# Performance work log

Measured on AMD Instinct MI355X. Metric: run time of the kernel, lower is better.

The kernel has to match this reference:

```python
import jax, jax.numpy as jnp
import numpy as np

N = 4096
BATCH = 8192


def setup_inputs() -> dict:
    key = jax.random.key(0)
    x = jax.random.normal(key, (BATCH, N), dtype=jnp.float32)
    return {"x": x}


def reference(x):
    # Radix-2 butterfly network (Fast Walsh-Hadamard Transform):
    # at stage s, positions i and i ^ (2**s) are combined as (a+b, a-b).
    B, n = x.shape
    num_stages = int(np.log2(n))
    r = x
    for stage in range(num_stages):  # fixed small loop over log2(n) stages
        stride = 2 ** stage
        # pairs (i, i+stride) live in blocks of 2*stride
        r4 = r.reshape(B, n // (2 * stride), 2, stride)
        a = r4[:, :, 0, :]
        b = r4[:, :, 1, :]
        r = jnp.stack([a + b, a - b], axis=2).reshape(B, n)
    return r
```

## Files before the change

### kernel.cpp

```cpp
#include <hip/hip_runtime.h>


#define N 4096

__device__ __forceinline__ void h16(float r[16]) {
    #pragma unroll
    for (int s = 1; s < 16; s <<= 1) {
        #pragma unroll
        for (int m = 0; m < 16; ++m) {
            if (!(m & s)) {
                float x = r[m], y = r[m ^ s];
                r[m]     = x + y;
                r[m ^ s] = x - y;
            }
        }
    }
}

__global__ __launch_bounds__(256, 8) void fwht4096_kernel(const float* __restrict__ in,
                                                          float* __restrict__ out) {
    __shared__ float lds[N];

    const int t = threadIdx.x;
    const long long row = blockIdx.x;
    const float* __restrict__ rowIn  = in  + row * (long long)N;
    float* __restrict__       rowOut = out + row * (long long)N;

    float r[16];

    #pragma unroll
    for (int j = 0; j < 4; ++j) {
        const float4 v = *reinterpret_cast<const float4*>(rowIn + t * 16 + j * 4);
        r[j * 4 + 0] = v.x; r[j * 4 + 1] = v.y;
        r[j * 4 + 2] = v.z; r[j * 4 + 3] = v.w;
    }

    h16(r);

    const int x = (t >> 4) & 1;
    const int s = (t >> 1) & 3;
    float* wbase = &lds[16 * (t ^ x)];
    #pragma unroll
    for (int c = 0; c < 4; ++c) {
        const int i0 = 4 * (c ^ s);
        const float4 v = make_float4(r[i0], r[i0 + 1], r[i0 + 2], r[i0 + 3]);
        *reinterpret_cast<float4*>(wbase + 4 * c) = v;
    }
    __syncthreads();

    {
        const int chi = t >> 4, a = t & 15;
        const int base = 256 * chi + a;
        const int fx = (chi & 1) << 4;
        #pragma unroll
        for (int k = 0; k < 16; ++k)
            r[k] = lds[(base + 16 * k) ^ fx ^ (((k >> 1) & 3) << 2)];
        h16(r);
        #pragma unroll
        for (int k = 0; k < 16; ++k)
            lds[(base + 16 * k) ^ fx ^ (((k >> 1) & 3) << 2)] = r[k];
    }
    __syncthreads();

    {
        const int b = t >> 4, a = t & 15;
        const int base = 16 * b + a;
        const int fb = ((b >> 1) & 3) << 2;
        #pragma unroll
        for (int k = 0; k < 16; ++k)
            r[k] = lds[(256 * k + base) ^ ((k & 1) << 4) ^ fb];
        h16(r);
        #pragma unroll
        for (int k = 0; k < 16; ++k)
            rowOut[k * 256 + t] = r[k];
    }
}

extern "C" void kernel_launch(void* const* d_in, const int* in_sizes, int n_in,
                              void* d_out, int out_size, void* d_ws, size_t ws_size,
                              hipStream_t stream) {
    const float* x = (const float*)d_in[0];
    float* y = (float*)d_out;
    const int rows = in_sizes[0] / N;
    fwht4096_kernel<<<rows, 256, 0, stream>>>(x, y);
}
```

Measured before the change: 228.2 us.

## Process four rows per block with register prefetch of next row

Each block now handles four rows in sequence and loads the next row's input into a second register set while the current row is transformed, so global load latency overlaps with compute. Barriers are replaced by a custom LDS-only waitcnt plus s_barrier, which avoids waiting on outstanding global loads, and the LDS swizzle indexing is precomputed. In exchange the grid is four times smaller, register pressure rises with the extra 16-float buffer, and the launch assumes rows divide evenly by four.

```diff
diff --git a/kernel.cpp b/kernel.cpp
--- a/kernel.cpp
+++ b/kernel.cpp
@@ -1,7 +1,8 @@
 #include <hip/hip_runtime.h>
 
 
-#define N 4096
+#define NN 4096
+#define RPB 4
 
 __device__ __forceinline__ void h16(float r[16]) {
     #pragma unroll
@@ -17,62 +18,76 @@
     }
 }
 
+__device__ __forceinline__ void lgkm_barrier() {
+    asm volatile("s_waitcnt lgkmcnt(0)" ::: "memory");
+    __builtin_amdgcn_s_barrier();
+    asm volatile("" ::: "memory");
+}
+
 __global__ __launch_bounds__(256, 8) void fwht4096_kernel(const float* __restrict__ in,
                                                           float* __restrict__ out) {
-    __shared__ float lds[N];
+    __shared__ float lds[NN];
 
-    const int t = threadIdx.x;
-    const long long row = blockIdx.x;
-    const float* __restrict__ rowIn  = in  + row * (long long)N;
-    float* __restrict__       rowOut = out + row * (long long)N;
+    const int t   = threadIdx.x;
+    const int chi = t >> 4;
 
-    float r[16];
+    const int wbase = (16 * t) ^ ((t & 7) << 2) ^ (((t >> 4) & 1) << 4);
+    const int tb    = (256 * chi + (t & 15)) ^ ((chi & 1) << 4);
+    const int tc    = t ^ ((chi & 7) << 2);
+
+    const long long row0 = (long long)blockIdx.x * RPB;
+    const float* __restrict__ pin = in + row0 * NN + t * 16;
+
+    float r[16], rn[16];
 
     #pragma unroll
     for (int j = 0; j < 4; ++j) {
-        const float4 v = *reinterpret_cast<const float4*>(rowIn + t * 16 + j * 4);
-        r[j * 4 + 0] = v.x; r[j * 4 + 1] = v.y;
-        r[j * 4 + 2] = v.z; r[j * 4 + 3] = v.w;
+        const float4 v = *reinterpret_cast<const float4*>(pin + 4 * j);
+        r[4*j+0] = v.x; r[4*j+1] = v.y; r[4*j+2] = v.z; r[4*j+3] = v.w;
     }
 
-    h16(r);
+    for (int it = 0; it < RPB; ++it) {
+        if (it + 1 < RPB) {
+            const float* __restrict__ pn = pin + (long long)(it + 1) * NN;
+            #pragma unroll
+            for (int j = 0; j < 4; ++j) {
+                const float4 v = *reinterpret_cast<const float4*>(pn + 4 * j);
+                rn[4*j+0] = v.x; rn[4*j+1] = v.y; rn[4*j+2] = v.z; rn[4*j+3] = v.w;
+            }
+        }
 
-    const int x = (t >> 4) & 1;
-    const int s = (t >> 1) & 3;
-    float* wbase = &lds[16 * (t ^ x)];
-    #pragma unroll
-    for (int c = 0; c < 4; ++c) {
-        const int i0 = 4 * (c ^ s);
-        const float4 v = make_float4(r[i0], r[i0 + 1], r[i0 + 2], r[i0 + 3]);
-        *reinterpret_cast<float4*>(wbase + 4 * c) = v;
-    }
-    __syncthreads();
+        h16(r);
+        #pragma unroll
+        for (int c = 0; c < 4; ++c) {
+            *reinterpret_cast<float4*>(&lds[wbase ^ (4 * c)]) =
+                make_float4(r[4*c], r[4*c+1], r[4*c+2], r[4*c+3]);
+        }
+        lgkm_barrier();
 
-    {
-        const int chi = t >> 4, a = t & 15;
-        const int base = 256 * chi + a;
-        const int fx = (chi & 1) << 4;
         #pragma unroll
         for (int k = 0; k < 16; ++k)
-            r[k] = lds[(base + 16 * k) ^ fx ^ (((k >> 1) & 3) << 2)];
+            r[k] = lds[tb ^ ((16 * k) ^ ((k & 7) << 2))];
         h16(r);
         #pragma unroll
         for (int k = 0; k < 16; ++k)
-            lds[(base + 16 * k) ^ fx ^ (((k >> 1) & 3) << 2)] = r[k];
-    }
-    __syncthreads();
+            lds[tb ^ ((16 * k) ^ ((k & 7) << 2))] = r[k];
+        lgkm_barrier();
 
-    {
-        const int b = t >> 4, a = t & 15;
-        const int base = 16 * b + a;
-        const int fb = ((b >> 1) & 3) << 2;
         #pragma unroll
         for (int k = 0; k < 16; ++k)
-            r[k] = lds[(256 * k + base) ^ ((k & 1) << 4) ^ fb];
+            r[k] = lds[tc ^ ((256 * k) ^ ((k & 1) << 4))];
         h16(r);
+
+        float* __restrict__ po = out + (row0 + it) * NN;
         #pragma unroll
         for (int k = 0; k < 16; ++k)
-            rowOut[k * 256 + t] = r[k];
+            po[k * 256 + t] = r[k];
+
+        if (it + 1 < RPB) {
+            lgkm_barrier();
+            #pragma unroll
+            for (int i = 0; i < 16; ++i) r[i] = rn[i];
+        }
     }
 }
 
@@ -81,6 +96,7 @@
                               hipStream_t stream) {
     const float* x = (const float*)d_in[0];
     float* y = (float*)d_out;
-    const int rows = in_sizes[0] / N;
-    fwht4096_kernel<<<rows, 256, 0, stream>>>(x, y);
+    const int rows = in_sizes[0] / NN;
+    const int blocks = rows / RPB;
+    fwht4096_kernel<<<blocks, 256, 0, stream>>>(x, y);
 }
```

New measurement: 252.3 us. 1.11x slower.
